# Optimization experiments

Measured on AMD Instinct MI355X. Metric: run time of the kernel, lower is better.

Reference implementation:

```python
import jax, jax.numpy as jnp
import numpy as np

N0, N1, N2, N3 = 200000, 50000, 12000, 3000
E0, E1, E2 = 500000, 120000, 30000
D_IN, D_H, D_OUT = 256, 256, 64


def setup_inputs() -> dict:
    key = jax.random.key(0)
    ks = jax.random.split(key, 16)
    s = 1.0 / np.sqrt(D_IN)
    return {
        "x": jax.random.normal(ks[0], (N0, D_IN), jnp.float32),
        "src0": jax.random.randint(ks[1], (E0,), 0, N0),
        "dst0": jax.random.randint(ks[2], (E0,), 0, N1),
        "src1": jax.random.randint(ks[3], (E1,), 0, N1),
        "dst1": jax.random.randint(ks[4], (E1,), 0, N2),
        "src2": jax.random.randint(ks[5], (E2,), 0, N2),
        "dst2": jax.random.randint(ks[6], (E2,), 0, N3),
        "num_dst0": N1, "num_dst1": N2, "num_dst2": N3,
        "Ws0": jax.random.normal(ks[7], (D_IN, D_H), jnp.float32) * s,
        "Wn0": jax.random.normal(ks[8], (D_IN, D_H), jnp.float32) * s,
        "b0": jnp.zeros((D_H,), jnp.float32),
        "Ws1": jax.random.normal(ks[9], (D_H, D_H), jnp.float32) * s,
        "Wn1": jax.random.normal(ks[10], (D_H, D_H), jnp.float32) * s,
        "b1": jnp.zeros((D_H,), jnp.float32),
        "Ws2": jax.random.normal(ks[11], (D_H, D_OUT), jnp.float32) * s,
        "Wn2": jax.random.normal(ks[12], (D_H, D_OUT), jnp.float32) * s,
        "b2": jnp.zeros((D_OUT,), jnp.float32),
    }


def sage_conv(src, dst, num_dst, h_src, Wn, Ws, b):
    # DGL SAGEConv(mean): fc_self(h_dst) + fc_neigh(mean_{in-edges} h_src) + bias
    h_dst = h_src[:num_dst]
    msg = h_src[src]                                          # [E, d] gather
    agg = jax.ops.segment_sum(msg, dst, num_segments=num_dst)  # [num_dst, d]
    deg = jax.ops.segment_sum(jnp.ones((dst.shape[0],), h_src.dtype), dst,
                              num_segments=num_dst)
    h_neigh = agg / jnp.maximum(deg, 1.0)[:, None]
    return h_dst @ Ws + h_neigh @ Wn + b


def reference(x, src0, dst0, src1, dst1, src2, dst2,
              num_dst0, num_dst1, num_dst2,
              Ws0, Wn0, b0, Ws1, Wn1, b1, Ws2, Wn2, b2):
    h = sage_conv(src0, dst0, num_dst0, x, Wn0, Ws0, b0)       # layer 0 (no act, per source)
    h = sage_conv(src1, dst1, num_dst1, h, Wn1, Ws1, b1)       # layer 1
    h = jax.nn.relu(h)                                         # activation after middle layer
    # dropout omitted (eval / deterministic mode)
    h = sage_conv(src2, dst2, num_dst2, h, Wn2, Ws2, b2)       # layer 2
    return h
```

## Files before the change

### kernel.cpp

```cpp
#include <hip/hip_runtime.h>

#define N0_SRC 200000
#define N1_DST 50000
#define N2_DST 12000
#define N3_DST 3000
#define NTOT_DST 65000
#define DH 256
#define DOUT 64
#define EMAX_TOT 650000

typedef __attribute__((ext_vector_type(8))) short short8;
typedef __attribute__((ext_vector_type(4))) float f32x4;

__device__ __forceinline__ ushort f2bf(float f) {
    union { float f; uint32_t u; } v; v.f = f;
    uint32_t r = (v.u + 0x7FFF + ((v.u >> 16) & 1)) >> 16;
    return (ushort)r;
}
__device__ __forceinline__ float bf2f(ushort u) {
    union { uint32_t u; float f; } v; v.u = ((uint32_t)u) << 16;
    return v.f;
}

__device__ __forceinline__ void gload16(const ushort* g, ushort* l) {
    __builtin_amdgcn_global_load_lds(
        (const __attribute__((address_space(1))) unsigned int*)g,
        (__attribute__((address_space(3))) unsigned int*)l,
        16, 0, 0);
}

__global__ void f32_to_bf16_kernel(const float* __restrict__ in,
                                   ushort* __restrict__ out, long n) {
    long i = ((long)blockIdx.x * 256 + threadIdx.x) * 4;
    if (i >= n) return;
    float4 v = *(const float4*)(in + i);
    ushort4 o;
    o.x = f2bf(v.x); o.y = f2bf(v.y); o.z = f2bf(v.z); o.w = f2bf(v.w);
    *(ushort4*)(out + i) = o;
}

__global__ void transpose_w_all(const float* __restrict__ W0, const float* __restrict__ W1,
                                const float* __restrict__ W2, const float* __restrict__ W3,
                                const float* __restrict__ W4, const float* __restrict__ W5,
                                ushort* __restrict__ out, int* __restrict__ cnt) {
    if (blockIdx.y == 0) {
        int z = blockIdx.x * 256 + threadIdx.x;
        if (z < NTOT_DST) cnt[z] = 0;
    }
    const float* W; int Ndim; ushort* o;
    switch (blockIdx.y) {
        case 0: W = W0; Ndim = 256; o = out; break;
        case 1: W = W1; Ndim = 256; o = out + 65536; break;
        case 2: W = W2; Ndim = 256; o = out + 131072; break;
        case 3: W = W3; Ndim = 256; o = out + 196608; break;
        case 4: W = W4; Ndim = 64;  o = out + 262144; break;
        default: W = W5; Ndim = 64; o = out + 278528; break;
    }
    int id = blockIdx.x * 256 + threadIdx.x;
    int n = id >> 8;
    int k = id & 255;
    if (n >= Ndim) return;
    o[id] = f2bf(W[k * Ndim + n]);
}

__global__ void hist3_kernel(const int* __restrict__ d0, int E0,
                             const int* __restrict__ d1, int E1,
                             const int* __restrict__ d2, int E2,
                             int* __restrict__ cnt) {
    int layer = blockIdx.y;
    const int* dst; int E; int base;
    if (layer == 0)      { dst = d0; E = E0; base = 0; }
    else if (layer == 1) { dst = d1; E = E1; base = N1_DST; }
    else                 { dst = d2; E = E2; base = N1_DST + N2_DST; }
    int e = blockIdx.x * 256 + threadIdx.x;
    if (e < E) atomicAdd(&cnt[base + dst[e]], 1);
}

__global__ void fill3_kernel(const int* __restrict__ s0, const int* __restrict__ d0, int E0,
                             const int* __restrict__ s1, const int* __restrict__ d1, int E1,
                             const int* __restrict__ s2, const int* __restrict__ d2, int E2,
                             int* __restrict__ cursor, int* __restrict__ eidx) {
    int layer = blockIdx.y;
    const int* src; const int* dst; int E; int base;
    if (layer == 0)      { src = s0; dst = d0; E = E0; base = 0; }
    else if (layer == 1) { src = s1; dst = d1; E = E1; base = N1_DST; }
    else                 { src = s2; dst = d2; E = E2; base = N1_DST + N2_DST; }
    int e = blockIdx.x * 256 + threadIdx.x;
    if (e < E) {
        int p = atomicAdd(&cursor[base + dst[e]], 1);
        eidx[p] = src[e];
    }
}

__global__ void scan_phase_a(const int* __restrict__ cnt, int* __restrict__ partial, int n) {
    __shared__ int red[4];
    int t = threadIdx.x;
    int i = blockIdx.x * 1024 + t * 4;
    int s = 0;
    if (i + 3 < n) {
        int4 v = *(const int4*)(cnt + i);
        s = v.x + v.y + v.z + v.w;
    }
#pragma unroll
    for (int d = 32; d; d >>= 1) s += __shfl_down(s, d, 64);
    if ((t & 63) == 0) red[t >> 6] = s;
    __syncthreads();
    if (t == 0) partial[blockIdx.x] = red[0] + red[1] + red[2] + red[3];
}

__global__ void scan_phase_b(int* __restrict__ partial, int nb) {
    int t = threadIdx.x;
    int own = (t < nb) ? partial[t] : 0;
    int v = own;
#pragma unroll
    for (int d = 1; d < 64; d <<= 1) {
        int u = __shfl_up(v, d, 64);
        if (t >= d) v += u;
    }
    if (t < nb) partial[t] = v - own;
}

__global__ void scan_phase_c(const int* __restrict__ cnt, const int* __restrict__ partial,
                             int* __restrict__ off, int* __restrict__ cursor, int n) {
    __shared__ int tsum[256];
    int t = threadIdx.x;
    int i = blockIdx.x * 1024 + t * 4;
    int4 c = make_int4(0, 0, 0, 0);
    if (i + 3 < n) c = *(const int4*)(cnt + i);
    int s = c.x + c.y + c.z + c.w;
    tsum[t] = s;
    __syncthreads();
#pragma unroll
    for (int d = 1; d < 256; d <<= 1) {
        int u = (t >= d) ? tsum[t - d] : 0;
        __syncthreads();
        tsum[t] += u;
        __syncthreads();
    }
    int base = partial[blockIdx.x] + tsum[t] - s;
    if (i + 3 < n) {
        int4 ov;
        ov.x = base;
        ov.y = ov.x + c.x;
        ov.z = ov.y + c.y;
        ov.w = ov.z + c.z;
        *(int4*)(off + i) = ov;
        *(int4*)(cursor + i) = ov;
        if (i + 4 == n) off[n] = ov.w + c.w;
    }
}

__global__ void gather_mean_bf16_kernel(const ushort* __restrict__ h,
                                        const int* __restrict__ off,
                                        const int* __restrict__ eidx,
                                        ushort* __restrict__ hn,
                                        int num_dst) {
    int w = blockIdx.x * 4 + (threadIdx.x >> 6);
    int lane = threadIdx.x & 63;
    if (w >= num_dst) return;
    int beg = off[w];
    int end = off[w + 1];
    float a0 = 0.f, a1 = 0.f, a2 = 0.f, a3 = 0.f;
    for (int i = beg; i < end; i += 4) {
        int rem = end - i;
        int j1 = i + (rem > 1 ? 1 : 0);
        int j2 = i + (rem > 2 ? 2 : 0);
        int j3 = i + (rem > 3 ? 3 : 0);
        float m1 = rem > 1 ? 1.f : 0.f;
        float m2 = rem > 2 ? 1.f : 0.f;
        float m3 = rem > 3 ? 1.f : 0.f;
        int s0 = eidx[i], s1 = eidx[j1], s2 = eidx[j2], s3 = eidx[j3];
        ushort4 v0 = ((const ushort4*)(h + (size_t)s0 * DH))[lane];
        ushort4 v1 = ((const ushort4*)(h + (size_t)s1 * DH))[lane];
        ushort4 v2 = ((const ushort4*)(h + (size_t)s2 * DH))[lane];
        ushort4 v3 = ((const ushort4*)(h + (size_t)s3 * DH))[lane];
        a0 += bf2f(v0.x) + m1 * bf2f(v1.x) + m2 * bf2f(v2.x) + m3 * bf2f(v3.x);
        a1 += bf2f(v0.y) + m1 * bf2f(v1.y) + m2 * bf2f(v2.y) + m3 * bf2f(v3.y);
        a2 += bf2f(v0.z) + m1 * bf2f(v1.z) + m2 * bf2f(v2.z) + m3 * bf2f(v3.z);
        a3 += bf2f(v0.w) + m1 * bf2f(v1.w) + m2 * bf2f(v2.w) + m3 * bf2f(v3.w);
    }
    float inv = 1.0f / fmaxf((float)(end - beg), 1.0f);
    ushort4 o;
    o.x = f2bf(a0 * inv); o.y = f2bf(a1 * inv);
    o.z = f2bf(a2 * inv); o.w = f2bf(a3 * inv);
    *(ushort4*)(hn + (size_t)w * DH + lane * 4) = o;
}

template <int MT, int NT, bool RELU, bool OUT_BF16>
__global__ __launch_bounds__(256) void gemm_dual(const ushort* __restrict__ Ad,
                                                 const ushort* __restrict__ An,
                                                 const ushort* __restrict__ Wst,
                                                 const ushort* __restrict__ Wnt,
                                                 const float* __restrict__ bias,
                                                 void* __restrict__ Cv,
                                                 int M, int N) {
    const int K = 256;
    const int BM = MT * 64;
    const int BN = NT * 16;
    __shared__ __align__(16) ushort lds[(2 * BM + 2 * BN) * 32];
    ushort* Asd = lds;
    ushort* Asn = lds + BM * 32;
    ushort* Bss = lds + 2 * BM * 32;
    ushort* Bsn = lds + 2 * BM * 32 + BN * 32;

    int tid  = threadIdx.x;
    int lane = tid & 63;
    int wid  = tid >> 6;
    int q    = lane >> 4;
    int mr   = lane & 15;
    int row0 = blockIdx.y * BM;
    int col0 = blockIdx.x * BN;

    f32x4 acc[MT][NT];
#pragma unroll
    for (int i = 0; i < MT; ++i)
#pragma unroll
        for (int j = 0; j < NT; ++j) acc[i][j] = (f32x4){0.f, 0.f, 0.f, 0.f};

    for (int k0 = 0; k0 < K; k0 += 32) {
#pragma unroll
        for (int c = 0; c < MT; ++c) {
            int chunk = c * 256 + tid;
            int r   = chunk >> 2;
            int sg  = (chunk & 3) ^ ((r >> 1) & 3);
            int row = row0 + r;
            if (row > M - 1) row = M - 1;
            const ushort* gd = Ad + (size_t)row * K + k0 + sg * 8;
            const ushort* gn = An + (size_t)row * K + k0 + sg * 8;
            int cb = (c * 256 + (tid & ~63)) * 8;
            gload16(gd, Asd + cb);
            gload16(gn, Asn + cb);
        }
#pragma unroll
        for (int c = 0; c < NT / 4; ++c) {
            int chunk = c * 256 + tid;
            int r  = chunk >> 2;
            int sg = (chunk & 3) ^ ((r >> 1) & 3);
            const ushort* gs = Wst + (size_t)(col0 + r) * K + k0 + sg * 8;
            const ushort* gw = Wnt + (size_t)(col0 + r) * K + k0 + sg * 8;
            int cb = (c * 256 + (tid & ~63)) * 8;
            gload16(gs, Bss + cb);
            gload16(gw, Bsn + cb);
        }
        __syncthreads();

        short8 ad[MT], an[MT];
#pragma unroll
        for (int mt = 0; mt < MT; ++mt) {
            int rho = wid * (MT * 16) + mt * 16 + mr;
            int o   = rho * 32 + ((q ^ ((rho >> 1) & 3)) * 8);
            ad[mt] = *(const short8*)(Asd + o);
            an[mt] = *(const short8*)(Asn + o);
        }
#pragma unroll
        for (int nt = 0; nt < NT; ++nt) {
            int rho = nt * 16 + mr;
            int o   = rho * 32 + ((q ^ ((rho >> 1) & 3)) * 8);
            short8 bs = *(const short8*)(Bss + o);
            short8 bn = *(const short8*)(Bsn + o);
#pragma unroll
            for (int mt = 0; mt < MT; ++mt) {
                acc[mt][nt] = __builtin_amdgcn_mfma_f32_16x16x32_bf16(
                    ad[mt], bs, acc[mt][nt], 0, 0, 0);
                acc[mt][nt] = __builtin_amdgcn_mfma_f32_16x16x32_bf16(
                    an[mt], bn, acc[mt][nt], 0, 0, 0);
            }
        }
        __syncthreads();
    }

#pragma unroll
    for (int mt = 0; mt < MT; ++mt) {
#pragma unroll
        for (int i = 0; i < 4; ++i) {
            int row = row0 + wid * (MT * 16) + mt * 16 + q * 4 + i;
            if (row >= M) continue;
#pragma unroll
            for (int nt = 0; nt < NT; ++nt) {
                int col = col0 + nt * 16 + mr;
                float v = acc[mt][nt][i] + bias[col];
                if (RELU) v = fmaxf(v, 0.0f);
                if (OUT_BF16) ((ushort*)Cv)[(size_t)row * N + col] = f2bf(v);
                else          ((float*)Cv)[(size_t)row * N + col] = v;
            }
        }
    }
}

extern "C" void kernel_launch(void* const* d_in, const int* in_sizes, int n_in,
                              void* d_out, int out_size, void* d_ws, size_t ws_size,
                              hipStream_t stream) {
    const float* x    = (const float*)d_in[0];
    const int* src0   = (const int*)d_in[1];
    const int* dst0   = (const int*)d_in[2];
    const int* src1   = (const int*)d_in[3];
    const int* dst1   = (const int*)d_in[4];
    const int* src2   = (const int*)d_in[5];
    const int* dst2   = (const int*)d_in[6];
    const float* Ws0  = (const float*)d_in[10];
    const float* Wn0  = (const float*)d_in[11];
    const float* b0   = (const float*)d_in[12];
    const float* Ws1  = (const float*)d_in[13];
    const float* Wn1  = (const float*)d_in[14];
    const float* b1   = (const float*)d_in[15];
    const float* Ws2  = (const float*)d_in[16];
    const float* Wn2  = (const float*)d_in[17];
    const float* b2   = (const float*)d_in[18];
    float* out = (float*)d_out;

    int E0 = in_sizes[1];
    int E1 = in_sizes[3];
    int E2 = in_sizes[5];

    ushort* wsu  = (ushort*)d_ws;
    ushort* xb   = wsu;
    ushort* hn0b = xb   + (size_t)N0_SRC * DH;
    ushort* h1b  = hn0b + (size_t)N1_DST * DH;
    ushort* hn1b = h1b  + (size_t)N1_DST * DH;
    ushort* h2b  = hn1b + (size_t)N2_DST * DH;
    ushort* hn2b = h2b  + (size_t)N2_DST * DH;
    ushort* Wt   = hn2b + (size_t)N3_DST * DH;
    ushort* Ws0t = Wt;
    ushort* Wn0t = Wt + 65536;
    ushort* Ws1t = Wt + 131072;
    ushort* Wn1t = Wt + 196608;
    ushort* Ws2t = Wt + 262144;
    ushort* Wn2t = Wt + 278528;
    int* cnt     = (int*)(Wt + 294912);
    int* off     = cnt + NTOT_DST;
    int* cursor  = off + NTOT_DST + 4;
    int* eidx    = cursor + NTOT_DST;
    int* partial = eidx + EMAX_TOT;

    long nxb = (long)N0_SRC * DH;
    f32_to_bf16_kernel<<<(int)((nxb / 4 + 255) / 256), 256, 0, stream>>>(x, xb, nxb);
    transpose_w_all<<<dim3(256, 6), 256, 0, stream>>>(Ws0, Wn0, Ws1, Wn1, Ws2, Wn2, Wt, cnt);

    int Emax = max(max(E0, E1), E2);
    int nb = (NTOT_DST + 1023) / 1024;
    hist3_kernel<<<dim3((Emax + 255) / 256, 3), 256, 0, stream>>>(dst0, E0, dst1, E1, dst2, E2, cnt);
    scan_phase_a<<<nb, 256, 0, stream>>>(cnt, partial, NTOT_DST);
    scan_phase_b<<<1, 64, 0, stream>>>(partial, nb);
    scan_phase_c<<<nb, 256, 0, stream>>>(cnt, partial, off, cursor, NTOT_DST);
    fill3_kernel<<<dim3((Emax + 255) / 256, 3), 256, 0, stream>>>(
        src0, dst0, E0, src1, dst1, E1, src2, dst2, E2, cursor, eidx);

    const int* off0 = off;
    const int* off1 = off + N1_DST;
    const int* off2 = off + N1_DST + N2_DST;

    gather_mean_bf16_kernel<<<(N1_DST + 3) / 4, 256, 0, stream>>>(xb, off0, eidx, hn0b, N1_DST);
    gemm_dual<2, 8, false, true><<<dim3(DH / 128, (N1_DST + 127) / 128), 256, 0, stream>>>(
        xb, hn0b, Ws0t, Wn0t, b0, h1b, N1_DST, DH);

    gather_mean_bf16_kernel<<<(N2_DST + 3) / 4, 256, 0, stream>>>(h1b, off1, eidx, hn1b, N2_DST);
    gemm_dual<2, 8, true, true><<<dim3(DH / 128, (N2_DST + 127) / 128), 256, 0, stream>>>(
        h1b, hn1b, Ws1t, Wn1t, b1, h2b, N2_DST, DH);

    gather_mean_bf16_kernel<<<(N3_DST + 3) / 4, 256, 0, stream>>>(h2b, off2, eidx, hn2b, N3_DST);
    gemm_dual<1, 4, false, false><<<dim3(DOUT / 64, (N3_DST + 63) / 64), 256, 0, stream>>>(
        h2b, hn2b, Ws2t, Wn2t, b2, out, N3_DST, DOUT);
}
```

Baseline: 505.7 us.

## Convert only needed x rows, gather layer-0 from fp32, fuse prep kernels

```diff
diff --git a/kernel.cpp b/kernel.cpp
--- a/kernel.cpp
+++ b/kernel.cpp
@@ -9,6 +9,10 @@
 #define DOUT 64
 #define EMAX_TOT 650000
 
+#define CONV_BLOCKS 6250
+#define TRANS_BLOCKS 1536
+#define ZERO_BLOCKS 254
+
 typedef __attribute__((ext_vector_type(8))) short short8;
 typedef __attribute__((ext_vector_type(4))) float f32x4;
 
@@ -29,38 +33,46 @@
         16, 0, 0);
 }
 
-__global__ void f32_to_bf16_kernel(const float* __restrict__ in,
-                                   ushort* __restrict__ out, long n) {
-    long i = ((long)blockIdx.x * 256 + threadIdx.x) * 4;
-    if (i >= n) return;
-    float4 v = *(const float4*)(in + i);
-    ushort4 o;
-    o.x = f2bf(v.x); o.y = f2bf(v.y); o.z = f2bf(v.z); o.w = f2bf(v.w);
-    *(ushort4*)(out + i) = o;
-}
-
-__global__ void transpose_w_all(const float* __restrict__ W0, const float* __restrict__ W1,
-                                const float* __restrict__ W2, const float* __restrict__ W3,
-                                const float* __restrict__ W4, const float* __restrict__ W5,
-                                ushort* __restrict__ out, int* __restrict__ cnt) {
-    if (blockIdx.y == 0) {
-        int z = blockIdx.x * 256 + threadIdx.x;
-        if (z < NTOT_DST) cnt[z] = 0;
-    }
-    const float* W; int Ndim; ushort* o;
-    switch (blockIdx.y) {
-        case 0: W = W0; Ndim = 256; o = out; break;
-        case 1: W = W1; Ndim = 256; o = out + 65536; break;
-        case 2: W = W2; Ndim = 256; o = out + 131072; break;
-        case 3: W = W3; Ndim = 256; o = out + 196608; break;
-        case 4: W = W4; Ndim = 64;  o = out + 262144; break;
-        default: W = W5; Ndim = 64; o = out + 278528; break;
-    }
-    int id = blockIdx.x * 256 + threadIdx.x;
-    int n = id >> 8;
-    int k = id & 255;
-    if (n >= Ndim) return;
-    o[id] = f2bf(W[k * Ndim + n]);
+__global__ void prep_kernel(const float* __restrict__ x,
+                            const float* __restrict__ W0, const float* __restrict__ W1,
+                            const float* __restrict__ W2, const float* __restrict__ W3,
+                            const float* __restrict__ W4, const float* __restrict__ W5,
+                            ushort* __restrict__ Wt, int* __restrict__ cnt,
+                            ushort* __restrict__ xb50) {
+    int bid = blockIdx.x;
+    if (bid < CONV_BLOCKS) {
+        long i = ((long)bid * 256 + threadIdx.x) * 8;
+        float4 a = *(const float4*)(x + i);
+        float4 b = *(const float4*)(x + i + 4);
+        ushort4 o0, o1;
+        o0.x = f2bf(a.x); o0.y = f2bf(a.y); o0.z = f2bf(a.z); o0.w = f2bf(a.w);
+        o1.x = f2bf(b.x); o1.y = f2bf(b.y); o1.z = f2bf(b.z); o1.w = f2bf(b.w);
+        *(ushort4*)(xb50 + i) = o0;
+        *(ushort4*)(xb50 + i + 4) = o1;
+        return;
+    }
+    if (bid < CONV_BLOCKS + TRANS_BLOCKS) {
+        int tb = bid - CONV_BLOCKS;
+        int wy = tb >> 8;
+        int wx = tb & 255;
+        const float* W; int Ndim; ushort* o;
+        switch (wy) {
+            case 0: W = W0; Ndim = 256; o = Wt; break;
+            case 1: W = W1; Ndim = 256; o = Wt + 65536; break;
+            case 2: W = W2; Ndim = 256; o = Wt + 131072; break;
+            case 3: W = W3; Ndim = 256; o = Wt + 196608; break;
+            case 4: W = W4; Ndim = 64;  o = Wt + 262144; break;
+            default: W = W5; Ndim = 64; o = Wt + 278528; break;
+        }
+        int id = wx * 256 + threadIdx.x;
+        int n = id >> 8;
+        int k = id & 255;
+        if (n >= Ndim) return;
+        o[id] = f2bf(W[k * Ndim + n]);
+        return;
+    }
+    int z = (bid - CONV_BLOCKS - TRANS_BLOCKS) * 256 + threadIdx.x;
+    if (z < NTOT_DST) cnt[z] = 0;
 }
 
 __global__ void hist3_kernel(const int* __restrict__ d0, int E0,
@@ -108,22 +120,21 @@
     if (t == 0) partial[blockIdx.x] = red[0] + red[1] + red[2] + red[3];
 }
 
-__global__ void scan_phase_b(int* __restrict__ partial, int nb) {
-    int t = threadIdx.x;
-    int own = (t < nb) ? partial[t] : 0;
-    int v = own;
-#pragma unroll
-    for (int d = 1; d < 64; d <<= 1) {
-        int u = __shfl_up(v, d, 64);
-        if (t >= d) v += u;
-    }
-    if (t < nb) partial[t] = v - own;
-}
-
 __global__ void scan_phase_c(const int* __restrict__ cnt, const int* __restrict__ partial,
                              int* __restrict__ off, int* __restrict__ cursor, int n) {
     __shared__ int tsum[256];
+    __shared__ int pbase;
     int t = threadIdx.x;
+    if (t < 64) {
+        int own = partial[t];
+        int v = own;
+#pragma unroll
+        for (int d = 1; d < 64; d <<= 1) {
+            int u = __shfl_up(v, d, 64);
+            if (t >= d) v += u;
+        }
+        if (t == blockIdx.x) pbase = v - own;
+    }
     int i = blockIdx.x * 1024 + t * 4;
     int4 c = make_int4(0, 0, 0, 0);
     if (i + 3 < n) c = *(const int4*)(cnt + i);
@@ -137,7 +148,7 @@
         tsum[t] += u;
         __syncthreads();
     }
-    int base = partial[blockIdx.x] + tsum[t] - s;
+    int base = pbase + tsum[t] - s;
     if (i + 3 < n) {
         int4 ov;
         ov.x = base;
@@ -148,6 +159,42 @@
         *(int4*)(cursor + i) = ov;
         if (i + 4 == n) off[n] = ov.w + c.w;
     }
+}
+
+__global__ void gather_mean_f32_kernel(const float* __restrict__ h,
+                                       const int* __restrict__ off,
+                                       const int* __restrict__ eidx,
+                                       ushort* __restrict__ hn,
+                                       int num_dst) {
+    int w = blockIdx.x * 4 + (threadIdx.x >> 6);
+    int lane = threadIdx.x & 63;
+    if (w >= num_dst) return;
+    int beg = off[w];
+    int end = off[w + 1];
+    float a0 = 0.f, a1 = 0.f, a2 = 0.f, a3 = 0.f;
+    for (int i = beg; i < end; i += 4) {
+        int rem = end - i;
+        int j1 = i + (rem > 1 ? 1 : 0);
+        int j2 = i + (rem > 2 ? 2 : 0);
+        int j3 = i + (rem > 3 ? 3 : 0);
+        float m1 = rem > 1 ? 1.f : 0.f;
+        float m2 = rem > 2 ? 1.f : 0.f;
+        float m3 = rem > 3 ? 1.f : 0.f;
+        int s0 = eidx[i], s1 = eidx[j1], s2 = eidx[j2], s3 = eidx[j3];
+        float4 v0 = ((const float4*)(h + (size_t)s0 * DH))[lane];
+        float4 v1 = ((const float4*)(h + (size_t)s1 * DH))[lane];
+        float4 v2 = ((const float4*)(h + (size_t)s2 * DH))[lane];
+        float4 v3 = ((const float4*)(h + (size_t)s3 * DH))[lane];
+        a0 += v0.x + m1 * v1.x + m2 * v2.x + m3 * v3.x;
+        a1 += v0.y + m1 * v1.y + m2 * v2.y + m3 * v3.y;
+        a2 += v0.z + m1 * v1.z + m2 * v2.z + m3 * v3.z;
+        a3 += v0.w + m1 * v1.w + m2 * v2.w + m3 * v3.w;
+    }
+    float inv = 1.0f / fmaxf((float)(end - beg), 1.0f);
+    ushort4 o;
+    o.x = f2bf(a0 * inv); o.y = f2bf(a1 * inv);
+    o.z = f2bf(a2 * inv); o.w = f2bf(a3 * inv);
+    *(ushort4*)(hn + (size_t)w * DH + lane * 4) = o;
 }
 
 __global__ void gather_mean_bf16_kernel(const ushort* __restrict__ h,
@@ -259,12 +306,13 @@
             short8 bs = *(const short8*)(Bss + o);
             short8 bn = *(const short8*)(Bsn + o);
 #pragma unroll
-            for (int mt = 0; mt < MT; ++mt) {
+            for (int mt = 0; mt < MT; ++mt)
                 acc[mt][nt] = __builtin_amdgcn_mfma_f32_16x16x32_bf16(
                     ad[mt], bs, acc[mt][nt], 0, 0, 0);
+#pragma unroll
+            for (int mt = 0; mt < MT; ++mt)
                 acc[mt][nt] = __builtin_amdgcn_mfma_f32_16x16x32_bf16(
                     an[mt], bn, acc[mt][nt], 0, 0, 0);
-            }
         }
         __syncthreads();
     }
@@ -313,8 +361,8 @@
     int E2 = in_sizes[5];
 
     ushort* wsu  = (ushort*)d_ws;
-    ushort* xb   = wsu;
-    ushort* hn0b = xb   + (size_t)N0_SRC * DH;
+    ushort* xb50 = wsu;
+    ushort* hn0b = xb50 + (size_t)N1_DST * DH;
     ushort* h1b  = hn0b + (size_t)N1_DST * DH;
     ushort* hn1b = h1b  + (size_t)N1_DST * DH;
     ushort* h2b  = hn1b + (size_t)N2_DST * DH;
@@ -332,15 +380,13 @@
     int* eidx    = cursor + NTOT_DST;
     int* partial = eidx + EMAX_TOT;
 
-    long nxb = (long)N0_SRC * DH;
-    f32_to_bf16_kernel<<<(int)((nxb / 4 + 255) / 256), 256, 0, stream>>>(x, xb, nxb);
-    transpose_w_all<<<dim3(256, 6), 256, 0, stream>>>(Ws0, Wn0, Ws1, Wn1, Ws2, Wn2, Wt, cnt);
+    prep_kernel<<<CONV_BLOCKS + TRANS_BLOCKS + ZERO_BLOCKS, 256, 0, stream>>>(
+        x, Ws0, Wn0, Ws1, Wn1, Ws2, Wn2, Wt, cnt, xb50);
 
     int Emax = max(max(E0, E1), E2);
     int nb = (NTOT_DST + 1023) / 1024;
     hist3_kernel<<<dim3((Emax + 255) / 256, 3), 256, 0, stream>>>(dst0, E0, dst1, E1, dst2, E2, cnt);
     scan_phase_a<<<nb, 256, 0, stream>>>(cnt, partial, NTOT_DST);
-    scan_phase_b<<<1, 64, 0, stream>>>(partial, nb);
     scan_phase_c<<<nb, 256, 0, stream>>>(cnt, partial, off, cursor, NTOT_DST);
     fill3_kernel<<<dim3((Emax + 255) / 256, 3), 256, 0, stream>>>(
         src0, dst0, E0, src1, dst1, E1, src2, dst2, E2, cursor, eidx);
@@ -349,12 +395,12 @@
     const int* off1 = off + N1_DST;
     const int* off2 = off + N1_DST + N2_DST;
 
-    gather_mean_bf16_kernel<<<(N1_DST + 3) / 4, 256, 0, stream>>>(xb, off0, eidx, hn0b, N1_DST);
-    gemm_dual<2, 8, false, true><<<dim3(DH / 128, (N1_DST + 127) / 128), 256, 0, stream>>>(
-        xb, hn0b, Ws0t, Wn0t, b0, h1b, N1_DST, DH);
+    gather_mean_f32_kernel<<<(N1_DST + 3) / 4, 256, 0, stream>>>(x, off0, eidx, hn0b, N1_DST);
+    gemm_dual<2, 16, false, true><<<dim3(1, (N1_DST + 127) / 128), 256, 0, stream>>>(
+        xb50, hn0b, Ws0t, Wn0t, b0, h1b, N1_DST, DH);
 
     gather_mean_bf16_kernel<<<(N2_DST + 3) / 4, 256, 0, stream>>>(h1b, off1, eidx, hn1b, N2_DST);
-    gemm_dual<2, 8, true, true><<<dim3(DH / 128, (N2_DST + 127) / 128), 256, 0, stream>>>(
+    gemm_dual<2, 16, true, true><<<dim3(1, (N2_DST + 127) / 128), 256, 0, stream>>>(
         h1b, hn1b, Ws1t, Wn1t, b1, h2b, N2_DST, DH);
 
     gather_mean_bf16_kernel<<<(N3_DST + 3) / 4, 256, 0, stream>>>(h2b, off2, eidx, hn2b, N3_DST);
```

Result: no change. 507.5 us (+0.4%).

## Fuse gather-mean into GEMM per layer and merge CSR prep into cooperative kernel

Applied to the files above, without the earlier changes.

```diff
diff --git a/kernel.cpp b/kernel.cpp
--- a/kernel.cpp
+++ b/kernel.cpp
@@ -1,4 +1,7 @@
 #include <hip/hip_runtime.h>
+#include <hip/hip_cooperative_groups.h>
+
+namespace cg = cooperative_groups;
 
 #define N0_SRC 200000
 #define N1_DST 50000
@@ -29,259 +32,239 @@
         16, 0, 0);
 }
 
-__global__ void f32_to_bf16_kernel(const float* __restrict__ in,
-                                   ushort* __restrict__ out, long n) {
-    long i = ((long)blockIdx.x * 256 + threadIdx.x) * 4;
-    if (i >= n) return;
-    float4 v = *(const float4*)(in + i);
-    ushort4 o;
-    o.x = f2bf(v.x); o.y = f2bf(v.y); o.z = f2bf(v.z); o.w = f2bf(v.w);
-    *(ushort4*)(out + i) = o;
-}
-
-__global__ void transpose_w_all(const float* __restrict__ W0, const float* __restrict__ W1,
-                                const float* __restrict__ W2, const float* __restrict__ W3,
-                                const float* __restrict__ W4, const float* __restrict__ W5,
-                                ushort* __restrict__ out, int* __restrict__ cnt) {
-    if (blockIdx.y == 0) {
-        int z = blockIdx.x * 256 + threadIdx.x;
-        if (z < NTOT_DST) cnt[z] = 0;
-    }
-    const float* W; int Ndim; ushort* o;
-    switch (blockIdx.y) {
-        case 0: W = W0; Ndim = 256; o = out; break;
-        case 1: W = W1; Ndim = 256; o = out + 65536; break;
-        case 2: W = W2; Ndim = 256; o = out + 131072; break;
-        case 3: W = W3; Ndim = 256; o = out + 196608; break;
-        case 4: W = W4; Ndim = 64;  o = out + 262144; break;
-        default: W = W5; Ndim = 64; o = out + 278528; break;
-    }
-    int id = blockIdx.x * 256 + threadIdx.x;
-    int n = id >> 8;
-    int k = id & 255;
-    if (n >= Ndim) return;
-    o[id] = f2bf(W[k * Ndim + n]);
-}
-
-__global__ void hist3_kernel(const int* __restrict__ d0, int E0,
-                             const int* __restrict__ d1, int E1,
-                             const int* __restrict__ d2, int E2,
-                             int* __restrict__ cnt) {
-    int layer = blockIdx.y;
-    const int* dst; int E; int base;
-    if (layer == 0)      { dst = d0; E = E0; base = 0; }
-    else if (layer == 1) { dst = d1; E = E1; base = N1_DST; }
-    else                 { dst = d2; E = E2; base = N1_DST + N2_DST; }
-    int e = blockIdx.x * 256 + threadIdx.x;
-    if (e < E) atomicAdd(&cnt[base + dst[e]], 1);
-}
-
-__global__ void fill3_kernel(const int* __restrict__ s0, const int* __restrict__ d0, int E0,
-                             const int* __restrict__ s1, const int* __restrict__ d1, int E1,
-                             const int* __restrict__ s2, const int* __restrict__ d2, int E2,
-                             int* __restrict__ cursor, int* __restrict__ eidx) {
-    int layer = blockIdx.y;
-    const int* src; const int* dst; int E; int base;
-    if (layer == 0)      { src = s0; dst = d0; E = E0; base = 0; }
-    else if (layer == 1) { src = s1; dst = d1; E = E1; base = N1_DST; }
-    else                 { src = s2; dst = d2; E = E2; base = N1_DST + N2_DST; }
-    int e = blockIdx.x * 256 + threadIdx.x;
-    if (e < E) {
-        int p = atomicAdd(&cursor[base + dst[e]], 1);
-        eidx[p] = src[e];
-    }
-}
-
-__global__ void scan_phase_a(const int* __restrict__ cnt, int* __restrict__ partial, int n) {
+struct PrepArgs {
+    const float* x;
+    const float* W[6];
+    const int* s0; const int* d0; int E0;
+    const int* s1; const int* d1; int E1;
+    const int* s2; const int* d2; int E2;
+    ushort* Wt; ushort* xb50;
+    int* cnt; int* off; int* cursor; int* eidx; int* partial;
+};
+
+__global__ __launch_bounds__(256) void prep_csr_kernel(PrepArgs a) {
+    cg::grid_group grid = cg::this_grid();
     __shared__ int red[4];
-    int t = threadIdx.x;
-    int i = blockIdx.x * 1024 + t * 4;
-    int s = 0;
-    if (i + 3 < n) {
-        int4 v = *(const int4*)(cnt + i);
-        s = v.x + v.y + v.z + v.w;
-    }
-#pragma unroll
-    for (int d = 32; d; d >>= 1) s += __shfl_down(s, d, 64);
-    if ((t & 63) == 0) red[t >> 6] = s;
+    __shared__ int tsum[256];
+    __shared__ int pbase;
+    const int GT = 256 * 256;
+    int gt = blockIdx.x * 256 + threadIdx.x;
+    int t  = threadIdx.x;
+
+    for (int i = gt; i < NTOT_DST; i += GT) a.cnt[i] = 0;
+    {
+        const float4* xv = (const float4*)a.x;
+        ushort4* xo = (ushort4*)a.xb50;
+        const int nv = N1_DST * DH / 4;
+        for (int i = gt; i < nv; i += GT) {
+            float4 v = xv[i];
+            ushort4 o;
+            o.x = f2bf(v.x); o.y = f2bf(v.y); o.z = f2bf(v.z); o.w = f2bf(v.w);
+            xo[i] = o;
+        }
+    }
+    for (int i = gt; i < 294912; i += GT) {
+        const float* W; ushort* o; int id; int Ndim;
+        if (i < 262144) { int wy = i >> 16; id = i & 65535; W = a.W[wy]; o = a.Wt + (wy << 16); Ndim = 256; }
+        else { int j = i - 262144; int wy = j >> 14; id = j & 16383; W = a.W[4 + wy]; o = a.Wt + 262144 + (wy << 14); Ndim = 64; }
+        int n = id >> 8, k = id & 255;
+        o[id] = f2bf(W[k * Ndim + n]);
+    }
+    grid.sync();
+
+    for (int e = gt; e < a.E0; e += GT) atomicAdd(&a.cnt[a.d0[e]], 1);
+    for (int e = gt; e < a.E1; e += GT) atomicAdd(&a.cnt[N1_DST + a.d1[e]], 1);
+    for (int e = gt; e < a.E2; e += GT) atomicAdd(&a.cnt[N1_DST + N2_DST + a.d2[e]], 1);
+    grid.sync();
+
+    if (blockIdx.x < 64) {
+        int i = blockIdx.x * 1024 + t * 4;
+        int s = 0;
+        if (i + 3 < NTOT_DST) {
+            int4 v = *(const int4*)(a.cnt + i);
+            s = v.x + v.y + v.z + v.w;
+        }
+#pragma unroll
+        for (int d = 32; d; d >>= 1) s += __shfl_down(s, d, 64);
+        if ((t & 63) == 0) red[t >> 6] = s;
+        __syncthreads();
+        if (t == 0) a.partial[blockIdx.x] = red[0] + red[1] + red[2] + red[3];
+    }
+    grid.sync();
+
+    if (blockIdx.x < 64) {
+        if (t < 64) {
+            int own = a.partial[t];
+            int v = own;
+#pragma unroll
+            for (int d = 1; d < 64; d <<= 1) {
+                int u = __shfl_up(v, d, 64);
+                if (t >= d) v += u;
+            }
+            if (t == (int)blockIdx.x) pbase = v - own;
+        }
+        int i = blockIdx.x * 1024 + t * 4;
+        int4 c = make_int4(0, 0, 0, 0);
+        if (i + 3 < NTOT_DST) c = *(const int4*)(a.cnt + i);
+        int s = c.x + c.y + c.z + c.w;
+        tsum[t] = s;
+        __syncthreads();
+#pragma unroll
+        for (int d = 1; d < 256; d <<= 1) {
+            int u = (t >= d) ? tsum[t - d] : 0;
+            __syncthreads();
+            tsum[t] += u;
+            __syncthreads();
+        }
+        int base = pbase + tsum[t] - s;
+        if (i + 3 < NTOT_DST) {
+            int4 ov;
+            ov.x = base;
+            ov.y = ov.x + c.x;
+            ov.z = ov.y + c.y;
+            ov.w = ov.z + c.z;
+            *(int4*)(a.off + i) = ov;
+            *(int4*)(a.cursor + i) = ov;
+            if (i + 4 == NTOT_DST) a.off[NTOT_DST] = ov.w + c.w;
+        }
+    }
+    grid.sync();
+
+    for (int e = gt; e < a.E0; e += GT) { int p = atomicAdd(&a.cursor[a.d0[e]], 1); a.eidx[p] = a.s0[e]; }
+    for (int e = gt; e < a.E1; e += GT) { int p = atomicAdd(&a.cursor[N1_DST + a.d1[e]], 1); a.eidx[p] = a.s1[e]; }
+    for (int e = gt; e < a.E2; e += GT) { int p = atomicAdd(&a.cursor[N1_DST + N2_DST + a.d2[e]], 1); a.eidx[p] = a.s2[e]; }
+}
+
+template <int NT, bool SRCF32, bool RELU, bool OUTBF>
+__global__ __launch_bounds__(256) void fused_layer(
+    const void* __restrict__ Hg,
+    const ushort* __restrict__ As,
+    const int* __restrict__ off, const int* __restrict__ eidx,
+    const ushort* __restrict__ Wst, const ushort* __restrict__ Wnt,
+    const float* __restrict__ bias, void* __restrict__ Cv,
+    int M, int N) {
+    const int K = 256;
+    const int BN = NT * 64;
+    const int LDA = 264;
+    __shared__ __align__(16) ushort AnS[64 * LDA];
+    __shared__ __align__(16) ushort AsS[64 * 32];
+    __shared__ __align__(16) ushort BsS[2 * BN * 32];
+    ushort* Bss = BsS;
+    ushort* Bsn = BsS + BN * 32;
+
+    int tid = threadIdx.x, lane = tid & 63, wid = tid >> 6;
+    int q = lane >> 4, mr = lane & 15;
+    int row0 = blockIdx.x * 64;
+
+    for (int rr = 0; rr < 16; ++rr) {
+        int rho = wid * 16 + rr;
+        int w = row0 + rho;
+        float a0 = 0.f, a1 = 0.f, a2 = 0.f, a3 = 0.f;
+        int deg = 0;
+        if (w < M) {
+            int beg = off[w], end = off[w + 1];
+            deg = end - beg;
+            for (int i = beg; i < end; i += 4) {
+                int rem = end - i;
+                int j1 = i + (rem > 1 ? 1 : 0);
+                int j2 = i + (rem > 2 ? 2 : 0);
+                int j3 = i + (rem > 3 ? 3 : 0);
+                float m1 = rem > 1 ? 1.f : 0.f;
+                float m2 = rem > 2 ? 1.f : 0.f;
+                float m3 = rem > 3 ? 1.f : 0.f;
+                int s0 = eidx[i], s1 = eidx[j1], s2 = eidx[j2], s3 = eidx[j3];
+                if (SRCF32) {
+                    const float4* h = (const float4*)Hg;
+                    float4 v0 = h[(size_t)s0 * 64 + lane];
+                    float4 v1 = h[(size_t)s1 * 64 + lane];
+                    float4 v2 = h[(size_t)s2 * 64 + lane];
+                    float4 v3 = h[(size_t)s3 * 64 + lane];
+                    a0 += v0.x + m1 * v1.x + m2 * v2.x + m3 * v3.x;
+                    a1 += v0.y + m1 * v1.y + m2 * v2.y + m3 * v3.y;
+                    a2 += v0.z + m1 * v1.z + m2 * v2.z + m3 * v3.z;
+                    a3 += v0.w + m1 * v1.w + m2 * v2.w + m3 * v3.w;
+                } else {
+                    const ushort4* h = (const ushort4*)Hg;
+                    ushort4 v0 = h[(size_t)s0 * 64 + lane];
+                    ushort4 v1 = h[(size_t)s1 * 64 + lane];
+                    ushort4 v2 = h[(size_t)s2 * 64 + lane];
+                    ushort4 v3 = h[(size_t)s3 * 64 + lane];
+                    a0 += bf2f(v0.x) + m1 * bf2f(v1.x) + m2 * bf2f(v2.x) + m3 * bf2f(v3.x);
+                    a1 += bf2f(v0.y) + m1 * bf2f(v1.y) + m2 * bf2f(v2.y) + m3 * bf2f(v3.y);
+                    a2 += bf2f(v0.z) + m1 * bf2f(v1.z) + m2 * bf2f(v2.z) + m3 * bf2f(v3.z);
+                    a3 += bf2f(v0.w) + m1 * bf2f(v1.w) + m2 * bf2f(v2.w) + m3 * bf2f(v3.w);
+                }
+            }
+        }
+        float inv = 1.0f / fmaxf((float)deg, 1.0f);
+        ushort4 o;
+        o.x = f2bf(a0 * inv); o.y = f2bf(a1 * inv);
+        o.z = f2bf(a2 * inv); o.w = f2bf(a3 * inv);
+        *(ushort4*)(&AnS[rho * LDA + lane * 4]) = o;
+    }
     __syncthreads();
-    if (t == 0) partial[blockIdx.x] = red[0] + red[1] + red[2] + red[3];
-}
-
-__global__ void scan_phase_b(int* __restrict__ partial, int nb) {
-    int t = threadIdx.x;
-    int own = (t < nb) ? partial[t] : 0;
-    int v = own;
-#pragma unroll
-    for (int d = 1; d < 64; d <<= 1) {
-        int u = __shfl_up(v, d, 64);
-        if (t >= d) v += u;
-    }
-    if (t < nb) partial[t] = v - own;
-}
-
-__global__ void scan_phase_c(const int* __restrict__ cnt, const int* __restrict__ partial,
-                             int* __restrict__ off, int* __restrict__ cursor, int n) {
-    __shared__ int tsum[256];
-    int t = threadIdx.x;
-    int i = blockIdx.x * 1024 + t * 4;
-    int4 c = make_int4(0, 0, 0, 0);
-    if (i + 3 < n) c = *(const int4*)(cnt + i);
-    int s = c.x + c.y + c.z + c.w;
-    tsum[t] = s;
-    __syncthreads();
-#pragma unroll
-    for (int d = 1; d < 256; d <<= 1) {
-        int u = (t >= d) ? tsum[t - d] : 0;
-        __syncthreads();
-        tsum[t] += u;
-        __syncthreads();
-    }
-    int base = partial[blockIdx.x] + tsum[t] - s;
-    if (i + 3 < n) {
-        int4 ov;
-        ov.x = base;
-        ov.y = ov.x + c.x;
-        ov.z = ov.y + c.y;
-        ov.w = ov.z + c.z;
-        *(int4*)(off + i) = ov;
-        *(int4*)(cursor + i) = ov;
-        if (i + 4 == n) off[n] = ov.w + c.w;
-    }
-}
-
-__global__ void gather_mean_bf16_kernel(const ushort* __restrict__ h,
-                                        const int* __restrict__ off,
-                                        const int* __restrict__ eidx,
-                                        ushort* __restrict__ hn,
-                                        int num_dst) {
-    int w = blockIdx.x * 4 + (threadIdx.x >> 6);
-    int lane = threadIdx.x & 63;
-    if (w >= num_dst) return;
-    int beg = off[w];
-    int end = off[w + 1];
-    float a0 = 0.f, a1 = 0.f, a2 = 0.f, a3 = 0.f;
-    for (int i = beg; i < end; i += 4) {
-        int rem = end - i;
-        int j1 = i + (rem > 1 ? 1 : 0);
-        int j2 = i + (rem > 2 ? 2 : 0);
-        int j3 = i + (rem > 3 ? 3 : 0);
-        float m1 = rem > 1 ? 1.f : 0.f;
-        float m2 = rem > 2 ? 1.f : 0.f;
-        float m3 = rem > 3 ? 1.f : 0.f;
-        int s0 = eidx[i], s1 = eidx[j1], s2 = eidx[j2], s3 = eidx[j3];
-        ushort4 v0 = ((const ushort4*)(h + (size_t)s0 * DH))[lane];
-        ushort4 v1 = ((const ushort4*)(h + (size_t)s1 * DH))[lane];
-        ushort4 v2 = ((const ushort4*)(h + (size_t)s2 * DH))[lane];
-        ushort4 v3 = ((const ushort4*)(h + (size_t)s3 * DH))[lane];
-        a0 += bf2f(v0.x) + m1 * bf2f(v1.x) + m2 * bf2f(v2.x) + m3 * bf2f(v3.x);
-        a1 += bf2f(v0.y) + m1 * bf2f(v1.y) + m2 * bf2f(v2.y) + m3 * bf2f(v3.y);
-        a2 += bf2f(v0.z) + m1 * bf2f(v1.z) + m2 * bf2f(v2.z) + m3 * bf2f(v3.z);
-        a3 += bf2f(v0.w) + m1 * bf2f(v1.w) + m2 * bf2f(v2.w) + m3 * bf2f(v3.w);
-    }
-    float inv = 1.0f / fmaxf((float)(end - beg), 1.0f);
-    ushort4 o;
-    o.x = f2bf(a0 * inv); o.y = f2bf(a1 * inv);
-    o.z = f2bf(a2 * inv); o.w = f2bf(a3 * inv);
-    *(ushort4*)(hn + (size_t)w * DH + lane * 4) = o;
-}
-
-template <int MT, int NT, bool RELU, bool OUT_BF16>
-__global__ __launch_bounds__(256) void gemm_dual(const ushort* __restrict__ Ad,
-                                                 const ushort* __restrict__ An,
-                                                 const ushort* __restrict__ Wst,
-                                                 const ushort* __restrict__ Wnt,
-                                                 const float* __restrict__ bias,
-                                                 void* __restrict__ Cv,
-                                                 int M, int N) {
-    const int K = 256;
-    const int BM = MT * 64;
-    const int BN = NT * 16;
-    __shared__ __align__(16) ushort lds[(2 * BM + 2 * BN) * 32];
-    ushort* Asd = lds;
-    ushort* Asn = lds + BM * 32;
-    ushort* Bss = lds + 2 * BM * 32;
-    ushort* Bsn = lds + 2 * BM * 32 + BN * 32;
-
-    int tid  = threadIdx.x;
-    int lane = tid & 63;
-    int wid  = tid >> 6;
-    int q    = lane >> 4;
-    int mr   = lane & 15;
-    int row0 = blockIdx.y * BM;
-    int col0 = blockIdx.x * BN;
-
-    f32x4 acc[MT][NT];
-#pragma unroll
-    for (int i = 0; i < MT; ++i)
+
+    f32x4 acc[4][NT];
+#pragma unroll
+    for (int i = 0; i < 4; ++i)
 #pragma unroll
         for (int j = 0; j < NT; ++j) acc[i][j] = (f32x4){0.f, 0.f, 0.f, 0.f};
 
     for (int k0 = 0; k0 < K; k0 += 32) {
-#pragma unroll
-        for (int c = 0; c < MT; ++c) {
-            int chunk = c * 256 + tid;
-            int r   = chunk >> 2;
-            int sg  = (chunk & 3) ^ ((r >> 1) & 3);
+        {
+            int r = tid >> 2;
+            int sg = (tid & 3) ^ ((r >> 1) & 3);
             int row = row0 + r;
             if (row > M - 1) row = M - 1;
-            const ushort* gd = Ad + (size_t)row * K + k0 + sg * 8;
-            const ushort* gn = An + (size_t)row * K + k0 + sg * 8;
-            int cb = (c * 256 + (tid & ~63)) * 8;
-            gload16(gd, Asd + cb);
-            gload16(gn, Asn + cb);
-        }
-#pragma unroll
-        for (int c = 0; c < NT / 4; ++c) {
+            gload16(As + (size_t)row * K + k0 + sg * 8, AsS + (tid & ~63) * 8);
+        }
+#pragma unroll
+        for (int c = 0; c < NT; ++c) {
             int chunk = c * 256 + tid;
-            int r  = chunk >> 2;
+            int r = chunk >> 2;
             int sg = (chunk & 3) ^ ((r >> 1) & 3);
-            const ushort* gs = Wst + (size_t)(col0 + r) * K + k0 + sg * 8;
-            const ushort* gw = Wnt + (size_t)(col0 + r) * K + k0 + sg * 8;
-            int cb = (c * 256 + (tid & ~63)) * 8;
-            gload16(gs, Bss + cb);
-            gload16(gw, Bsn + cb);
+            gload16(Wst + (size_t)r * K + k0 + sg * 8, Bss + (c * 256 + (tid & ~63)) * 8);
+            gload16(Wnt + (size_t)r * K + k0 + sg * 8, Bsn + (c * 256 + (tid & ~63)) * 8);
         }
         __syncthreads();
 
-        short8 ad[MT], an[MT];
-#pragma unroll
-        for (int mt = 0; mt < MT; ++mt) {
-            int rho = wid * (MT * 16) + mt * 16 + mr;
-            int o   = rho * 32 + ((q ^ ((rho >> 1) & 3)) * 8);
-            ad[mt] = *(const short8*)(Asd + o);
-            an[mt] = *(const short8*)(Asn + o);
+        short8 av[4], aw[4];
+#pragma unroll
+        for (int mt = 0; mt < 4; ++mt) {
+            int rho = mt * 16 + mr;
+            av[mt] = *(const short8*)(AsS + rho * 32 + ((q ^ ((rho >> 1) & 3)) * 8));
+            aw[mt] = *(const short8*)(AnS + rho * LDA + k0 + q * 8);
         }
 #pragma unroll
         for (int nt = 0; nt < NT; ++nt) {
-            int rho = nt * 16 + mr;
-            int o   = rho * 32 + ((q ^ ((rho >> 1) & 3)) * 8);
-            short8 bs = *(const short8*)(Bss + o);
-            short8 bn = *(const short8*)(Bsn + o);
-#pragma unroll
-            for (int mt = 0; mt < MT; ++mt) {
+            int rb = wid * (NT * 16) + nt * 16 + mr;
+            int ob = rb * 32 + ((q ^ ((rb >> 1) & 3)) * 8);
+            short8 bs = *(const short8*)(Bss + ob);
+            short8 bn = *(const short8*)(Bsn + ob);
+#pragma unroll
+            for (int mt = 0; mt < 4; ++mt) {
                 acc[mt][nt] = __builtin_amdgcn_mfma_f32_16x16x32_bf16(
-                    ad[mt], bs, acc[mt][nt], 0, 0, 0);
+                    av[mt], bs, acc[mt][nt], 0, 0, 0);
                 acc[mt][nt] = __builtin_amdgcn_mfma_f32_16x16x32_bf16(
-                    an[mt], bn, acc[mt][nt], 0, 0, 0);
+                    aw[mt], bn, acc[mt][nt], 0, 0, 0);
             }
         }
         __syncthreads();
     }
 
 #pragma unroll
-    for (int mt = 0; mt < MT; ++mt) {
+    for (int mt = 0; mt < 4; ++mt) {
 #pragma unroll
         for (int i = 0; i < 4; ++i) {
-            int row = row0 + wid * (MT * 16) + mt * 16 + q * 4 + i;
+            int row = row0 + mt * 16 + q * 4 + i;
             if (row >= M) continue;
 #pragma unroll
             for (int nt = 0; nt < NT; ++nt) {
-                int col = col0 + nt * 16 + mr;
+                int col = wid * (NT * 16) + nt * 16 + mr;
                 float v = acc[mt][nt][i] + bias[col];
                 if (RELU) v = fmaxf(v, 0.0f);
-                if (OUT_BF16) ((ushort*)Cv)[(size_t)row * N + col] = f2bf(v);
-                else          ((float*)Cv)[(size_t)row * N + col] = v;
+                if (OUTBF) ((ushort*)Cv)[(size_t)row * N + col] = f2bf(v);
+                else       ((float*)Cv)[(size_t)row * N + col] = v;
             }
         }
     }
@@ -313,13 +296,10 @@
     int E2 = in_sizes[5];
 
     ushort* wsu  = (ushort*)d_ws;
-    ushort* xb   = wsu;
-    ushort* hn0b = xb   + (size_t)N0_SRC * DH;
-    ushort* h1b  = hn0b + (size_t)N1_DST * DH;
-    ushort* hn1b = h1b  + (size_t)N1_DST * DH;
-    ushort* h2b  = hn1b + (size_t)N2_DST * DH;
-    ushort* hn2b = h2b  + (size_t)N2_DST * DH;
-    ushort* Wt   = hn2b + (size_t)N3_DST * DH;
+    ushort* xb50 = wsu;
+    ushort* h1b  = xb50 + (size_t)N1_DST * DH;
+    ushort* h2b  = h1b  + (size_t)N1_DST * DH;
+    ushort* Wt   = h2b  + (size_t)N2_DST * DH;
     ushort* Ws0t = Wt;
     ushort* Wn0t = Wt + 65536;
     ushort* Ws1t = Wt + 131072;
@@ -332,32 +312,30 @@
     int* eidx    = cursor + NTOT_DST;
     int* partial = eidx + EMAX_TOT;
 
-    long nxb = (long)N0_SRC * DH;
-    f32_to_bf16_kernel<<<(int)((nxb / 4 + 255) / 256), 256, 0, stream>>>(x, xb, nxb);
-    transpose_w_all<<<dim3(256, 6), 256, 0, stream>>>(Ws0, Wn0, Ws1, Wn1, Ws2, Wn2, Wt, cnt);
-
-    int Emax = max(max(E0, E1), E2);
-    int nb = (NTOT_DST + 1023) / 1024;
-    hist3_kernel<<<dim3((Emax + 255) / 256, 3), 256, 0, stream>>>(dst0, E0, dst1, E1, dst2, E2, cnt);
-    scan_phase_a<<<nb, 256, 0, stream>>>(cnt, partial, NTOT_DST);
-    scan_phase_b<<<1, 64, 0, stream>>>(partial, nb);
-    scan_phase_c<<<nb, 256, 0, stream>>>(cnt, partial, off, cursor, NTOT_DST);
-    fill3_kernel<<<dim3((Emax + 255) / 256, 3), 256, 0, stream>>>(
-        src0, dst0, E0, src1, dst1, E1, src2, dst2, E2, cursor, eidx);
+    PrepArgs pa;
+    pa.x = x;
+    pa.W[0] = Ws0; pa.W[1] = Wn0; pa.W[2] = Ws1;
+    pa.W[3] = Wn1; pa.W[4] = Ws2; pa.W[5] = Wn2;
+    pa.s0 = src0; pa.d0 = dst0; pa.E0 = E0;
+    pa.s1 = src1; pa.d1 = dst1; pa.E1 = E1;
+    pa.s2 = src2; pa.d2 = dst2; pa.E2 = E2;
+    pa.Wt = Wt; pa.xb50 = xb50;
+    pa.cnt = cnt; pa.off = off; pa.cursor = cursor;
+    pa.eidx = eidx; pa.partial = partial;
+    void* kargs[] = { &pa };
+    hipLaunchCooperativeKernel((void*)prep_csr_kernel, dim3(256), dim3(256),
+                               kargs, 0, stream);
 
     const int* off0 = off;
     const int* off1 = off + N1_DST;
     const int* off2 = off + N1_DST + N2_DST;
 
-    gather_mean_bf16_kernel<<<(N1_DST + 3) / 4, 256, 0, stream>>>(xb, off0, eidx, hn0b, N1_DST);
-    gemm_dual<2, 8, false, true><<<dim3(DH / 128, (N1_DST + 127) / 128), 256, 0, stream>>>(
-        xb, hn0b, Ws0t, Wn0t, b0, h1b, N1_DST, DH);
-
-    gather_mean_bf16_kernel<<<(N2_DST + 3) / 4, 256, 0, stream>>>(h1b, off1, eidx, hn1b, N2_DST);
-    gemm_dual<2, 8, true, true><<<dim3(DH / 128, (N2_DST + 127) / 128), 256, 0, stream>>>(
-        h1b, hn1b, Ws1t, Wn1t, b1, h2b, N2_DST, DH);
-
-    gather_mean_bf16_kernel<<<(N3_DST + 3) / 4, 256, 0, stream>>>(h2b, off2, eidx, hn2b, N3_DST);
-    gemm_dual<1, 4, false, false><<<dim3(DOUT / 64, (N3_DST + 63) / 64), 256, 0, stream>>>(
-        h2b, hn2b, Ws2t, Wn2t, b2, out, N3_DST, DOUT);
-}
+    fused_layer<4, true, false, true><<<(N1_DST + 63) / 64, 256, 0, stream>>>(
+        x, xb50, off0, eidx, Ws0t, Wn0t, b0, h1b, N1_DST, DH);
+
+    fused_layer<4, false, true, true><<<(N2_DST + 63) / 64, 256, 0, stream>>>(
+        h1b, h1b, off1, eidx, Ws1t, Wn1t, b1, h2b, N2_DST, DH);
+
+    fused_layer<1, false, false, false><<<(N3_DST + 63) / 64, 256, 0, stream>>>(
+        h2b, h2b, off2, eidx, Ws2t, Wn2t, b2, out, N3_DST, DOUT);
+}
```

New measurement: 744.6 us. +47.2%, slower.
